# Performance work log

Measured on AMD Instinct MI355X. Metric: run time of the kernel, lower is better.

Reference implementation:

```python
import jax, jax.numpy as jnp
import numpy as np

D_MODEL = 2048
N_HEADS = 16
N_KV = 4
D_HEAD = D_MODEL // N_HEADS
N_GROUPS = N_HEADS // N_KV
THETA = 10000.0


def bitlinear(x, W):
    """BitNet b1.58 BitLinear: ternary weights (absmean scale) + 8-bit absmax activations (STE)."""
    sw = jnp.mean(jnp.abs(W)) + 1e-5
    Wq = jnp.clip(jnp.round(W / sw), -1.0, 1.0) * sw
    sx = 127.0 / jnp.clip(jnp.max(jnp.abs(x), axis=-1, keepdims=True), 1e-5, None)
    xq = jnp.clip(jnp.round(x * sx), -128.0, 127.0) / sx
    return jnp.einsum('bsd,od->bso', xq, Wq)


def rope_tables(seq, d_head, dtype=jnp.float32):
    freqs = 1.0 / (THETA ** (jnp.arange(0, d_head, 2, dtype=dtype) / d_head))
    t = jnp.arange(seq, dtype=dtype)
    ang = jnp.outer(t, freqs)  # [seq, d_head//2]
    return jnp.cos(ang), jnp.sin(ang)


def apply_rope(x, cos, sin):
    # x: [b, h, s, d]; cos/sin: [s, d//2] -> broadcast [1,1,s,d//2]
    c = cos[None, None]
    s = sin[None, None]
    x1, x2 = jnp.split(x, 2, axis=-1)
    return jnp.concatenate([x1 * c - x2 * s, x2 * c + x1 * s], axis=-1)


def setup_inputs() -> dict:
    key = jax.random.key(0)
    ks = jax.random.split(key, 5)
    return {
        'x': jax.random.normal(ks[0], (2, 2048, D_MODEL), jnp.float32),
        'Wq': jax.random.normal(ks[1], (D_MODEL, D_MODEL), jnp.float32) * 0.02,
        'Wk': jax.random.normal(ks[2], (N_KV * D_HEAD, D_MODEL), jnp.float32) * 0.02,
        'Wv': jax.random.normal(ks[3], (N_KV * D_HEAD, D_MODEL), jnp.float32) * 0.02,
        'Wo': jax.random.normal(ks[4], (D_MODEL, D_MODEL), jnp.float32) * 0.02,
    }


def reference(x, Wq, Wk, Wv, Wo):
    b, s, _ = x.shape
    q = bitlinear(x, Wq).reshape(b, s, N_HEADS, D_HEAD).transpose(0, 2, 1, 3)
    k = bitlinear(x, Wk).reshape(b, s, N_KV, D_HEAD).transpose(0, 2, 1, 3)
    v = bitlinear(x, Wv).reshape(b, s, N_KV, D_HEAD).transpose(0, 2, 1, 3)
    cos, sin = rope_tables(s, D_HEAD)
    q = apply_rope(q, cos, sin)
    k = apply_rope(k, cos, sin)
    # GQA without materializing expanded K/V: group query heads per kv head
    qg = q.reshape(b, N_KV, N_GROUPS, s, D_HEAD)
    scale = 1.0 / jnp.sqrt(jnp.asarray(D_HEAD, x.dtype))
    scores = jnp.einsum('bkgsd,bktd->bkgst', qg, k) * scale  # [b,kv,g,s,s]
    causal = jnp.triu(jnp.ones((s, s), dtype=bool), k=1)
    scores = jnp.where(causal[None, None, None], jnp.asarray(-jnp.inf, scores.dtype), scores)
    p = jax.nn.softmax(scores, axis=-1)
    out = jnp.einsum('bkgst,bktd->bkgsd', p, v)  # [b,kv,g,s,d]
    out = out.reshape(b, N_HEADS, s, D_HEAD).transpose(0, 2, 1, 3).reshape(b, s, D_MODEL)
    return bitlinear(out, Wo)
```

## Files before the change

kernel.cpp:

```cpp
#include <hip/hip_runtime.h>
#include <hip/hip_bf16.h>
#include <stdint.h>

typedef __bf16 bf16x8 __attribute__((ext_vector_type(8)));
typedef float f32x4 __attribute__((ext_vector_type(4)));
typedef int i32x4 __attribute__((ext_vector_type(4)));
typedef unsigned short u16x8 __attribute__((ext_vector_type(8)));
typedef unsigned short u16x4 __attribute__((ext_vector_type(4)));
typedef signed char i8x8 __attribute__((ext_vector_type(8)));
typedef signed char i8x4 __attribute__((ext_vector_type(4)));

__device__ __forceinline__ unsigned short f2bf(float f) {
  union { float f; unsigned int u; } v; v.f = f;
  unsigned int r = v.u + 0x7fffu + ((v.u >> 16) & 1u);
  return (unsigned short)(r >> 16);
}

__device__ __forceinline__ f32x4 mfma16(bf16x8 a, bf16x8 b, f32x4 c) {
  return __builtin_amdgcn_mfma_f32_16x16x32_bf16(a, b, c, 0, 0, 0);
}

__device__ __forceinline__ i32x4 mfma_i8(i32x4 a, i32x4 b, i32x4 c) {
  return __builtin_amdgcn_mfma_i32_16x16x64_i8(a, b, c, 0, 0, 0);
}

__device__ __forceinline__ void gload_lds16(const void* g, void* l) {
  __builtin_amdgcn_global_load_lds(
      (const __attribute__((address_space(1))) void*)g,
      (__attribute__((address_space(3))) void*)l, 16, 0, 0);
}

__global__ void absum_k(const float* __restrict__ w, long n4, float* __restrict__ out) {
  long i = (long)blockIdx.x * blockDim.x + threadIdx.x;
  long stride = (long)gridDim.x * blockDim.x;
  const float4* w4 = (const float4*)w;
  float s = 0.f;
  for (; i < n4; i += stride) {
    float4 v = w4[i];
    s += fabsf(v.x) + fabsf(v.y) + fabsf(v.z) + fabsf(v.w);
  }
  #pragma unroll
  for (int o = 32; o; o >>= 1) s += __shfl_down(s, o);
  __shared__ float sm[4];
  int lane = threadIdx.x & 63, wv = threadIdx.x >> 6;
  if (lane == 0) sm[wv] = s;
  __syncthreads();
  if (threadIdx.x == 0) atomicAdd(out, sm[0] + sm[1] + sm[2] + sm[3]);
}

__global__ void finalize_k(const float* __restrict__ sums, float* __restrict__ sw) {
  int i = threadIdx.x;
  if (i < 4) {
    const float inv[4] = {1.f/(2048.f*2048.f), 1.f/(512.f*2048.f),
                          1.f/(512.f*2048.f), 1.f/(2048.f*2048.f)};
    sw[i] = sums[i] * inv[i] + 1e-5f;
  }
}

__global__ void quantw_k(const float* __restrict__ w, signed char* __restrict__ o,
                         long n4, const float* __restrict__ swp) {
  float sw = *swp;
  long i = (long)blockIdx.x * blockDim.x + threadIdx.x;
  long stride = (long)gridDim.x * blockDim.x;
  const float4* w4 = (const float4*)w;
  i8x4* o4 = (i8x4*)o;
  for (; i < n4; i += stride) {
    float4 v = w4[i];
    i8x4 t;
    t[0] = (signed char)(int)fminf(fmaxf(rintf(v.x / sw), -1.f), 1.f);
    t[1] = (signed char)(int)fminf(fmaxf(rintf(v.y / sw), -1.f), 1.f);
    t[2] = (signed char)(int)fminf(fmaxf(rintf(v.z / sw), -1.f), 1.f);
    t[3] = (signed char)(int)fminf(fmaxf(rintf(v.w / sw), -1.f), 1.f);
    o4[i] = t;
  }
}

__global__ void ropetab_k(float* __restrict__ cosT, float* __restrict__ sinT) {
  int idx = blockIdx.x * 256 + threadIdx.x;
  int s = idx >> 6, d = idx & 63;
  float freq = expf(-(float)d * (9.210340371976184f / 64.0f));
  float ang = (float)s * freq;
  cosT[idx] = cosf(ang);
  sinT[idx] = sinf(ang);
}

__global__ __launch_bounds__(256) void quanta_k(const float* __restrict__ x,
                                                signed char* __restrict__ xq,
                                                float* __restrict__ rs) {
  int row = blockIdx.x;
  const float* xr = x + (size_t)row * 2048;
  int tid = threadIdx.x;
  float4 v0 = ((const float4*)xr)[tid * 2];
  float4 v1 = ((const float4*)xr)[tid * 2 + 1];
  float m = fmaxf(fmaxf(fmaxf(fabsf(v0.x), fabsf(v0.y)), fmaxf(fabsf(v0.z), fabsf(v0.w))),
                  fmaxf(fmaxf(fabsf(v1.x), fabsf(v1.y)), fmaxf(fabsf(v1.z), fabsf(v1.w))));
  #pragma unroll
  for (int o = 32; o; o >>= 1) m = fmaxf(m, __shfl_xor(m, o));
  __shared__ float sm[4];
  if ((tid & 63) == 0) sm[tid >> 6] = m;
  __syncthreads();
  m = fmaxf(fmaxf(sm[0], sm[1]), fmaxf(sm[2], sm[3]));
  float rm = fmaxf(m, 1e-5f);
  float sx = 127.0f / rm;
  float vv[8] = {v0.x, v0.y, v0.z, v0.w, v1.x, v1.y, v1.z, v1.w};
  i8x8 o8;
  #pragma unroll
  for (int j = 0; j < 8; j++) {
    float r = rintf(vv[j] * sx);
    r = fminf(fmaxf(r, -128.f), 127.f);
    o8[j] = (signed char)(int)r;
  }
  ((i8x8*)(xq + (size_t)row * 2048))[tid] = o8;
  if (tid == 0) rs[row] = rm * (1.0f / 127.0f);
}

__global__ __launch_bounds__(256) void gemm_k(const signed char* __restrict__ A,
                                              const signed char* __restrict__ Bt,
                                              float* __restrict__ C,
                                              int M, int N, int K,
                                              const float* __restrict__ rowscale,
                                              const float* __restrict__ sw, int mode) {
  __shared__ alignas(16) signed char As[128 * 64];
  __shared__ alignas(16) signed char Bs[128 * 64];
  int tid = threadIdx.x;
  int lane = tid & 63, wv = tid >> 6;
  int g = lane >> 4, li = lane & 15;
  int wm = wv >> 1, wn = wv & 1;
  int L = blockIdx.x + gridDim.x * blockIdx.y;
  int nwg = gridDim.x * gridDim.y;
  int swz_id = (L & 7) * (nwg >> 3) + (L >> 3);
  int m0 = (swz_id / gridDim.x) * 128, n0 = (swz_id % gridDim.x) * 128;
  int sr = lane >> 2;
  int sc = lane & 3;
  int gc = (sc ^ ((sr >> 1) & 3)) * 16;
  int swz = (g ^ ((li >> 1) & 3)) * 16;
  i32x4 acc[4][4] = {};

  for (int k0 = 0; k0 < K; k0 += 64) {
    __syncthreads();
    #pragma unroll
    for (int j = 0; j < 2; j++) {
      int row = (wv * 2 + j) * 16 + sr;
      gload_lds16(&A[(size_t)(m0 + row) * K + k0 + gc], &As[(wv * 2 + j) * 1024]);
      gload_lds16(&Bt[(size_t)(n0 + row) * K + k0 + gc], &Bs[(wv * 2 + j) * 1024]);
    }
    __syncthreads();
    i32x4 af[4], bfr[4];
    #pragma unroll
    for (int i = 0; i < 4; i++)
      af[i] = *(const i32x4*)&As[(wm * 64 + i * 16 + li) * 64 + swz];
    #pragma unroll
    for (int j = 0; j < 4; j++)
      bfr[j] = *(const i32x4*)&Bs[(wn * 64 + j * 16 + li) * 64 + swz];
    #pragma unroll
    for (int i = 0; i < 4; i++)
      #pragma unroll
      for (int j = 0; j < 4; j++)
        acc[i][j] = mfma_i8(af[i], bfr[j], acc[i][j]);
  }

  #pragma unroll
  for (int i = 0; i < 4; i++) {
    int row = m0 + wm * 64 + i * 16 + g * 4;
    #pragma unroll
    for (int j = 0; j < 4; j++) {
      int col = n0 + wn * 64 + j * 16 + li;
      float s = (mode == 0) ? ((col < 2048) ? sw[0] : (col < 2560 ? sw[1] : sw[2]))
                            : sw[3];
      #pragma unroll
      for (int r = 0; r < 4; r++)
        C[(size_t)(row + r) * N + col] = (float)acc[i][j][r] * (rowscale[row + r] * s);
    }
  }
}

__global__ __launch_bounds__(256) void ropeapply_k(const float* __restrict__ raw,
                                                   const float* __restrict__ cosT,
                                                   const float* __restrict__ sinT,
                                                   unsigned short* __restrict__ qb,
                                                   unsigned short* __restrict__ kb) {
  const float CS = 0.1275356234f;
  int r = blockIdx.x;
  int b = r >> 11, s = r & 2047;
  const float* row = raw + (size_t)r * 3072;
  int tid = threadIdx.x;
  for (int idx = tid; idx < 1024; idx += 256) {
    int h = idx >> 6, d = idx & 63;
    float x1 = row[h * 128 + d], x2 = row[h * 128 + d + 64];
    float c = cosT[s * 64 + d], sn = sinT[s * 64 + d];
    size_t base = ((size_t)(b * 16 + h) * 2048 + s) * 128;
    qb[base + d]      = f2bf((x1 * c - x2 * sn) * CS);
    qb[base + d + 64] = f2bf((x2 * c + x1 * sn) * CS);
  }
  {
    int h = tid >> 6, d = tid & 63;
    float x1 = row[2048 + h * 128 + d], x2 = row[2048 + h * 128 + d + 64];
    float c = cosT[s * 64 + d], sn = sinT[s * 64 + d];
    size_t base = ((size_t)(b * 4 + h) * 2048 + s) * 128;
    kb[base + d]      = f2bf(x1 * c - x2 * sn);
    kb[base + d + 64] = f2bf(x2 * c + x1 * sn);
  }
}

__global__ __launch_bounds__(256) void transv_k(const float* __restrict__ raw,
                                                unsigned short* __restrict__ vtb) {
  __shared__ unsigned short T[128][136];
  int sc = blockIdx.x, hk = blockIdx.y, b = blockIdx.z;
  int tid = threadIdx.x;
  #pragma unroll
  for (int i = 0; i < 16; i++) {
    int idx4 = i * 256 + tid;
    int s = idx4 >> 5, d4 = idx4 & 31;
    float4 v = *(const float4*)&raw[((size_t)(b * 2048 + sc * 128 + s)) * 3072 +
                                    2560 + hk * 128 + d4 * 4];
    u16x4 t4;
    t4[0] = f2bf(v.x); t4[1] = f2bf(v.y); t4[2] = f2bf(v.z); t4[3] = f2bf(v.w);
    *(u16x4*)&T[s][d4 * 4] = t4;
  }
  __syncthreads();
  int d = tid >> 1, s0 = (tid & 1) * 64;
  size_t obase = ((size_t)(b * 4 + hk) * 128 + d) * 2048 + sc * 128 + s0;
  #pragma unroll
  for (int j = 0; j < 8; j++) {
    u16x8 o8;
    #pragma unroll
    for (int e = 0; e < 8; e++) {
      int kvp = (j >> 2) * 32 + (e >> 2) * 16 + (j & 3) * 4 + (e & 3);
      o8[e] = T[s0 + kvp][d];
    }
    *(u16x8*)&vtb[obase + j * 8] = o8;
  }
}

__global__ __launch_bounds__(256) void attn_k(const unsigned short* __restrict__ qb,
                                              const unsigned short* __restrict__ kb,
                                              const unsigned short* __restrict__ vtb,
                                              float* __restrict__ out) {
  int gid = blockIdx.x;
  int tq = 31 - (gid >> 5);
  int hb = gid & 31;
  int h = hb & 15, b = hb >> 4;
  int wv = threadIdx.x >> 6, lane = threadIdx.x & 63;
  int g = lane >> 4, li = lane & 15;
  int kh = h >> 2;
  const unsigned short* qp = qb + ((size_t)(b * 16 + h) * 2048) * 128;
  const unsigned short* kp = kb + ((size_t)(b * 4 + kh) * 2048) * 128;
  const unsigned short* vp = vtb + ((size_t)(b * 4 + kh) * 128) * 2048;

  __shared__ unsigned short Ks[64 * 128];
  __shared__ unsigned short Vs[2][128 * 64];

  int qw = tq * 64 + wv * 16;
  int nt = tq + 1;
  bf16x8 qf[4];
  #pragma unroll
  for (int kk = 0; kk < 4; kk++)
    qf[kk] = *(const bf16x8*)&qp[(size_t)(qw + li) * 128 + kk * 32 + g * 8];
  f32x4 oacc[8] = {};
  float mrun = -INFINITY, lrun = 0.f;

  #define STAGE_K(T_) do {                                                  \
    int kv0_ = (T_) * 64;                                                   \
    _Pragma("unroll")                                                       \
    for (int i_ = 0; i_ < 4; i_++) {                                        \
      int r_ = wv * 16 + i_ * 4 + g;                                        \
      gload_lds16(kp + (size_t)(kv0_ + r_) * 128 + ((li ^ (r_ & 7)) * 8),   \
                  &Ks[(wv * 16 + i_ * 4) * 128]);                           \
    } } while (0)
  #define STAGE_V(T_, BUF_) do {                                            \
    int kv0_ = (T_) * 64;                                                   \
    _Pragma("unroll")                                                       \
    for (int i_ = 0; i_ < 4; i_++) {                                        \
      int d_ = wv * 32 + i_ * 8 + (lane >> 3);                              \
      gload_lds16(vp + (size_t)d_ * 2048 + kv0_ + (((lane & 7) ^ (d_ & 7)) * 8), \
                  &Vs[BUF_][(wv * 32 + i_ * 8) * 64]);                      \
    } } while (0)

  STAGE_K(0);
  STAGE_V(0, 0);
  if (nt > 1) STAGE_V(1, 1);

  #pragma unroll 1
  for (int t = 0; t < nt; ++t) {
    if (t == nt - 1) asm volatile("s_waitcnt vmcnt(0)" ::: "memory");
    else             asm volatile("s_waitcnt vmcnt(4)" ::: "memory");
    __builtin_amdgcn_s_barrier();
    asm volatile("" ::: "memory");

    f32x4 st[4] = {};
    __builtin_amdgcn_s_setprio(1);
    #pragma unroll
    for (int kk = 0; kk < 4; kk++) {
      #pragma unroll
      for (int n = 0; n < 4; n++) {
        bf16x8 kf = *(const bf16x8*)&Ks[(n * 16 + li) * 128 +
                                        (((kk * 4 + g) ^ (li & 7)) * 8)];
        st[n] = mfma16(kf, qf[kk], st[n]);
      }
    }
    __builtin_amdgcn_s_setprio(0);

    asm volatile("" ::: "memory");
    __builtin_amdgcn_s_barrier();
    asm volatile("" ::: "memory");
    if (t + 1 < nt) STAGE_K(t + 1);

    if (t == nt - 1) {
      int qrel = qw + li - t * 64;
      #pragma unroll
      for (int n = 0; n < 4; n++)
        #pragma unroll
        for (int r = 0; r < 4; r++)
          if ((n * 16 + g * 4 + r) > qrel) st[n][r] = -INFINITY;
    }
    float mx = st[0][0];
    #pragma unroll
    for (int n = 0; n < 4; n++)
      #pragma unroll
      for (int r = 0; r < 4; r++) mx = fmaxf(mx, st[n][r]);
    mx = fmaxf(mx, __shfl_xor(mx, 16));
    mx = fmaxf(mx, __shfl_xor(mx, 32));
    float mnew = fmaxf(mrun, mx);
    float alpha = exp2f(mrun - mnew);
    float lsum = 0.f;
    bf16x8 pa0, pa1;
    #pragma unroll
    for (int n = 0; n < 4; n++) {
      #pragma unroll
      for (int r = 0; r < 4; r++) {
        float p = exp2f(st[n][r] - mnew);
        lsum += p;
        if (n < 2) pa0[(n & 1) * 4 + r] = (__bf16)p;
        else       pa1[(n & 1) * 4 + r] = (__bf16)p;
      }
    }
    lsum += __shfl_xor(lsum, 16);
    lsum += __shfl_xor(lsum, 32);
    lrun = lrun * alpha + lsum;
    mrun = mnew;
    if (__any(alpha != 1.0f)) {
      float ar[4];
      #pragma unroll
      for (int r = 0; r < 4; r++) ar[r] = __shfl(alpha, g * 4 + r, 64);
      #pragma unroll
      for (int dn = 0; dn < 8; dn++)
        #pragma unroll
        for (int r = 0; r < 4; r++) oacc[dn][r] *= ar[r];
    }

    int cur = t & 1;
    __builtin_amdgcn_s_setprio(1);
    #pragma unroll
    for (int dn = 0; dn < 8; dn++) {
      int d = dn * 16 + li;
      bf16x8 vf0 = *(const bf16x8*)&Vs[cur][d * 64 + ((g ^ (li & 7)) * 8)];
      bf16x8 vf1 = *(const bf16x8*)&Vs[cur][d * 64 + (((4 + g) ^ (li & 7)) * 8)];
      oacc[dn] = mfma16(pa0, vf0, oacc[dn]);
      oacc[dn] = mfma16(pa1, vf1, oacc[dn]);
    }
    __builtin_amdgcn_s_setprio(0);

    asm volatile("" ::: "memory");
    __builtin_amdgcn_s_barrier();
    asm volatile("" ::: "memory");
    if (t + 2 < nt) STAGE_V(t + 2, cur);
  }
  #undef STAGE_K
  #undef STAGE_V

  float linv = 1.0f / lrun;
  float lr_[4];
  #pragma unroll
  for (int r = 0; r < 4; r++) lr_[r] = __shfl(linv, g * 4 + r, 64);
  size_t obase = ((size_t)(b * 2048 + qw + g * 4)) * 2048 + h * 128;
  #pragma unroll
  for (int dn = 0; dn < 8; dn++)
    #pragma unroll
    for (int r = 0; r < 4; r++)
      out[obase + (size_t)r * 2048 + dn * 16 + li] = oacc[dn][r] * lr_[r];
}

extern "C" void kernel_launch(void* const* d_in, const int* in_sizes, int n_in,
                              void* d_out, int out_size, void* d_ws, size_t ws_size,
                              hipStream_t stream) {
  const float* x  = (const float*)d_in[0];
  const float* Wq = (const float*)d_in[1];
  const float* Wk = (const float*)d_in[2];
  const float* Wv = (const float*)d_in[3];
  const float* Wo = (const float*)d_in[4];
  float* out = (float*)d_out;

  char* ws = (char*)d_ws;
  size_t off = 0;
  auto alloc = [&](size_t bytes) -> void* {
    void* p = ws + off;
    off = (off + bytes + 255) & ~(size_t)255;
    return p;
  };
  float* sums = (float*)alloc(16);
  float* sw   = (float*)alloc(16);
  float* rs   = (float*)alloc(4096 * 4);
  float* rs2  = (float*)alloc(4096 * 4);
  float* cosT = (float*)alloc((size_t)131072 * 4);
  float* sinT = (float*)alloc((size_t)131072 * 4);
  signed char* Wcat = (signed char*)alloc((size_t)3072 * 2048);
  signed char* Wot  = (signed char*)alloc((size_t)2048 * 2048);
  unsigned short* qb   = (unsigned short*)alloc((size_t)2 * 16 * 2048 * 128 * 2);
  unsigned short* kb   = (unsigned short*)alloc((size_t)2 * 4 * 2048 * 128 * 2);
  unsigned short* vtb  = (unsigned short*)alloc((size_t)2 * 4 * 128 * 2048 * 2);
  signed char* xq   = (signed char*)alloc((size_t)4096 * 2048);
  float* raw  = (float*)alloc((size_t)4096 * 3072 * 4);
  float* attn = raw;

  hipMemsetAsync(sums, 0, 16, stream);
  absum_k<<<256, 256, 0, stream>>>(Wq, (long)2048 * 2048 / 4, sums + 0);
  absum_k<<<128, 256, 0, stream>>>(Wk, (long)512 * 2048 / 4, sums + 1);
  absum_k<<<128, 256, 0, stream>>>(Wv, (long)512 * 2048 / 4, sums + 2);
  absum_k<<<256, 256, 0, stream>>>(Wo, (long)2048 * 2048 / 4, sums + 3);
  finalize_k<<<1, 4, 0, stream>>>(sums, sw);
  quantw_k<<<512, 256, 0, stream>>>(Wq, Wcat, (long)2048 * 2048 / 4, sw + 0);
  quantw_k<<<128, 256, 0, stream>>>(Wk, Wcat + (size_t)2048 * 2048, (long)512 * 2048 / 4, sw + 1);
  quantw_k<<<128, 256, 0, stream>>>(Wv, Wcat + (size_t)2560 * 2048, (long)512 * 2048 / 4, sw + 2);
  quantw_k<<<512, 256, 0, stream>>>(Wo, Wot, (long)2048 * 2048 / 4, sw + 3);
  ropetab_k<<<512, 256, 0, stream>>>(cosT, sinT);
  quanta_k<<<4096, 256, 0, stream>>>(x, xq, rs);
  dim3 g1(3072 / 128, 4096 / 128);
  gemm_k<<<g1, 256, 0, stream>>>(xq, Wcat, raw, 4096, 3072, 2048, rs, sw, 0);
  ropeapply_k<<<4096, 256, 0, stream>>>(raw, cosT, sinT, qb, kb);
  transv_k<<<dim3(16, 4, 2), 256, 0, stream>>>(raw, vtb);
  attn_k<<<1024, 256, 0, stream>>>(qb, kb, vtb, attn);
  quanta_k<<<4096, 256, 0, stream>>>(attn, xq, rs2);
  dim3 g2(2048 / 128, 4096 / 128);
  gemm_k<<<g2, 256, 0, stream>>>(xq, Wot, out, 4096, 2048, 2048, rs2, sw, 1);
}
```

Before: 323.6 us.

## Use 128-row query tiles with 8 waves and lazy softmax rescaling in attention

The attention kernel now runs 512 threads per block, each block covering 128 query rows with 8 waves that share every staged K/V tile, which halves the grid and doubles K/V reuse per load. The K/V staging loops are split across 8 waves with fewer loads per thread, and the causal mask is applied to every tile that crosses the diagonal. The online softmax now rescales only when the row max grows by more than a threshold, and the per-row sum reduction is deferred to the end to remove shuffles from the inner loop. The cost is lower occupancy per block, a coarser causal tail of work, and more reliance on the lazy-max bound for numerical safety.

```diff
diff --git a/kernel.cpp b/kernel.cpp
--- a/kernel.cpp
+++ b/kernel.cpp
@@ -232,12 +232,12 @@
   }
 }
 
-__global__ __launch_bounds__(256) void attn_k(const unsigned short* __restrict__ qb,
+__global__ __launch_bounds__(512) void attn_k(const unsigned short* __restrict__ qb,
                                               const unsigned short* __restrict__ kb,
                                               const unsigned short* __restrict__ vtb,
                                               float* __restrict__ out) {
   int gid = blockIdx.x;
-  int tq = 31 - (gid >> 5);
+  int tq = 15 - (gid >> 5);
   int hb = gid & 31;
   int h = hb & 15, b = hb >> 4;
   int wv = threadIdx.x >> 6, lane = threadIdx.x & 63;
@@ -250,8 +250,8 @@
   __shared__ unsigned short Ks[64 * 128];
   __shared__ unsigned short Vs[2][128 * 64];
 
-  int qw = tq * 64 + wv * 16;
-  int nt = tq + 1;
+  int qw = tq * 128 + wv * 16;
+  int nt = 2 * tq + 2;
   bf16x8 qf[4];
   #pragma unroll
   for (int kk = 0; kk < 4; kk++)
@@ -262,18 +262,20 @@
   #define STAGE_K(T_) do {                                                  \
     int kv0_ = (T_) * 64;                                                   \
     _Pragma("unroll")                                                       \
-    for (int i_ = 0; i_ < 4; i_++) {                                        \
-      int r_ = wv * 16 + i_ * 4 + g;                                        \
-      gload_lds16(kp + (size_t)(kv0_ + r_) * 128 + ((li ^ (r_ & 7)) * 8),   \
-                  &Ks[(wv * 16 + i_ * 4) * 128]);                           \
+    for (int i_ = 0; i_ < 2; i_++) {                                        \
+      int r_ = (wv * 2 + i_) * 4 + (lane >> 4);                             \
+      int c_ = lane & 15;                                                   \
+      gload_lds16(kp + (size_t)(kv0_ + r_) * 128 + ((c_ ^ (r_ & 7)) * 8),   \
+                  &Ks[(wv * 2 + i_) * 512]);                                \
     } } while (0)
   #define STAGE_V(T_, BUF_) do {                                            \
     int kv0_ = (T_) * 64;                                                   \
     _Pragma("unroll")                                                       \
-    for (int i_ = 0; i_ < 4; i_++) {                                        \
-      int d_ = wv * 32 + i_ * 8 + (lane >> 3);                              \
-      gload_lds16(vp + (size_t)d_ * 2048 + kv0_ + (((lane & 7) ^ (d_ & 7)) * 8), \
-                  &Vs[BUF_][(wv * 32 + i_ * 8) * 64]);                      \
+    for (int i_ = 0; i_ < 2; i_++) {                                        \
+      int d_ = (wv * 2 + i_) * 8 + (lane >> 3);                             \
+      int c_ = lane & 7;                                                    \
+      gload_lds16(vp + (size_t)d_ * 2048 + kv0_ + ((c_ ^ (d_ & 7)) * 8),    \
+                  &Vs[BUF_][(wv * 2 + i_) * 512]);                          \
     } } while (0)
 
   STAGE_K(0);
@@ -282,8 +284,9 @@
 
   #pragma unroll 1
   for (int t = 0; t < nt; ++t) {
+    int kv0 = t * 64;
     if (t == nt - 1) asm volatile("s_waitcnt vmcnt(0)" ::: "memory");
-    else             asm volatile("s_waitcnt vmcnt(4)" ::: "memory");
+    else             asm volatile("s_waitcnt vmcnt(2)" ::: "memory");
     __builtin_amdgcn_s_barrier();
     asm volatile("" ::: "memory");
 
@@ -305,48 +308,46 @@
     asm volatile("" ::: "memory");
     if (t + 1 < nt) STAGE_K(t + 1);
 
-    if (t == nt - 1) {
-      int qrel = qw + li - t * 64;
+    if (kv0 + 63 > qw) {
+      int qrel = qw + li - kv0;
       #pragma unroll
       for (int n = 0; n < 4; n++)
         #pragma unroll
         for (int r = 0; r < 4; r++)
           if ((n * 16 + g * 4 + r) > qrel) st[n][r] = -INFINITY;
     }
-    float mx = st[0][0];
-    #pragma unroll
-    for (int n = 0; n < 4; n++)
-      #pragma unroll
-      for (int r = 0; r < 4; r++) mx = fmaxf(mx, st[n][r]);
-    mx = fmaxf(mx, __shfl_xor(mx, 16));
-    mx = fmaxf(mx, __shfl_xor(mx, 32));
-    float mnew = fmaxf(mrun, mx);
-    float alpha = exp2f(mrun - mnew);
+    float mx = fmaxf(fmaxf(fmaxf(st[0][0], st[0][1]), fmaxf(st[0][2], st[0][3])),
+                     fmaxf(fmaxf(st[1][0], st[1][1]), fmaxf(st[1][2], st[1][3])));
+    mx = fmaxf(mx, fmaxf(fmaxf(fmaxf(st[2][0], st[2][1]), fmaxf(st[2][2], st[2][3])),
+                         fmaxf(fmaxf(st[3][0], st[3][1]), fmaxf(st[3][2], st[3][3]))));
+    if (!__all(mx - mrun <= 8.0f)) {
+      float rmx = fmaxf(mx, __shfl_xor(mx, 16));
+      rmx = fmaxf(rmx, __shfl_xor(rmx, 32));
+      float mnew = fmaxf(mrun, rmx);
+      float alpha = exp2f(mrun - mnew);
+      lrun *= alpha;
+      float ar[4];
+      #pragma unroll
+      for (int r = 0; r < 4; r++) ar[r] = __shfl(alpha, g * 4 + r, 64);
+      #pragma unroll
+      for (int dn = 0; dn < 8; dn++)
+        #pragma unroll
+        for (int r = 0; r < 4; r++) oacc[dn][r] *= ar[r];
+      mrun = mnew;
+    }
     float lsum = 0.f;
     bf16x8 pa0, pa1;
     #pragma unroll
     for (int n = 0; n < 4; n++) {
       #pragma unroll
       for (int r = 0; r < 4; r++) {
-        float p = exp2f(st[n][r] - mnew);
+        float p = exp2f(st[n][r] - mrun);
         lsum += p;
         if (n < 2) pa0[(n & 1) * 4 + r] = (__bf16)p;
         else       pa1[(n & 1) * 4 + r] = (__bf16)p;
       }
     }
-    lsum += __shfl_xor(lsum, 16);
-    lsum += __shfl_xor(lsum, 32);
-    lrun = lrun * alpha + lsum;
-    mrun = mnew;
-    if (__any(alpha != 1.0f)) {
-      float ar[4];
-      #pragma unroll
-      for (int r = 0; r < 4; r++) ar[r] = __shfl(alpha, g * 4 + r, 64);
-      #pragma unroll
-      for (int dn = 0; dn < 8; dn++)
-        #pragma unroll
-        for (int r = 0; r < 4; r++) oacc[dn][r] *= ar[r];
-    }
+    lrun += lsum;
 
     int cur = t & 1;
     __builtin_amdgcn_s_setprio(1);
@@ -368,6 +369,8 @@
   #undef STAGE_K
   #undef STAGE_V
 
+  lrun += __shfl_xor(lrun, 16);
+  lrun += __shfl_xor(lrun, 32);
   float linv = 1.0f / lrun;
   float lr_[4];
   #pragma unroll
@@ -428,7 +431,7 @@
   gemm_k<<<g1, 256, 0, stream>>>(xq, Wcat, raw, 4096, 3072, 2048, rs, sw, 0);
   ropeapply_k<<<4096, 256, 0, stream>>>(raw, cosT, sinT, qb, kb);
   transv_k<<<dim3(16, 4, 2), 256, 0, stream>>>(raw, vtb);
-  attn_k<<<1024, 256, 0, stream>>>(qb, kb, vtb, attn);
+  attn_k<<<512, 512, 0, stream>>>(qb, kb, vtb, attn);
   quanta_k<<<4096, 256, 0, stream>>>(attn, xq, rs2);
   dim3 g2(2048 / 128, 4096 / 128);
   gemm_k<<<g2, 256, 0, stream>>>(xq, Wot, out, 4096, 2048, 2048, rs2, sw, 1);
```

New measurement: 325.8 us. No clear change (+0.7%).
